# Performance work log

Measured on AMD Instinct MI355X. Metric: run time of the kernel, lower is better.

## Reference

```python
import math
import jax, jax.numpy as jnp
import numpy as np
from jax import lax

N = 224
EPS_BN = 1e-5


def _conv(x, w, b):
    y = lax.conv_general_dilated(x, w, (1, 1), 'SAME',
                                 dimension_numbers=('NCHW', 'OIHW', 'NCHW'))
    return y + b[None, :, None, None]


def _bn(x, g, beta, m, v):
    # eval-mode BatchNorm2d with running stats
    inv = lax.rsqrt(v + EPS_BN)
    return (x - m[None, :, None, None]) * (g * inv)[None, :, None, None] + beta[None, :, None, None]


def _maxpool2(x):
    return lax.reduce_window(x, -jnp.inf, lax.max, (1, 1, 2, 2), (1, 1, 2, 2), 'VALID')


def setup_inputs() -> dict:
    key = jax.random.key(0)
    ks = jax.random.split(key, 12)
    idx = np.arange(N, dtype=np.float32)
    angles = 2.0 * math.pi * idx[None, :] * idx[:, None] / N
    inp = {
        'sequences': jax.random.normal(ks[0], (16, 8, 3, N, N), dtype=jnp.float32),
        'dft_cos': jnp.asarray(np.cos(angles), dtype=jnp.float32),
        'dft_sin': jnp.asarray(np.sin(angles), dtype=jnp.float32),
        'conv1_w': jax.random.normal(ks[1], (16, 3, 3, 3), dtype=jnp.float32) * 0.1,
        'conv1_b': jnp.zeros((16,), jnp.float32),
        'bn1_g': jnp.ones((16,), jnp.float32),
        'bn1_b': jnp.zeros((16,), jnp.float32),
        'bn1_m': jnp.zeros((16,), jnp.float32),
        'bn1_v': jnp.ones((16,), jnp.float32),
        'conv2_w': jax.random.normal(ks[2], (32, 16, 3, 3), dtype=jnp.float32) * 0.05,
        'conv2_b': jnp.zeros((32,), jnp.float32),
        'bn2_g': jnp.ones((32,), jnp.float32),
        'bn2_b': jnp.zeros((32,), jnp.float32),
        'bn2_m': jnp.zeros((32,), jnp.float32),
        'bn2_v': jnp.ones((32,), jnp.float32),
        'conv3_w': jax.random.normal(ks[3], (64, 32, 3, 3), dtype=jnp.float32) * 0.05,
        'conv3_b': jnp.zeros((64,), jnp.float32),
        'bn3_g': jnp.ones((64,), jnp.float32),
        'bn3_b': jnp.zeros((64,), jnp.float32),
        'bn3_m': jnp.zeros((64,), jnp.float32),
        'bn3_v': jnp.ones((64,), jnp.float32),
        'fc_w': jax.random.normal(ks[4], (128, 64), dtype=jnp.float32) * 0.1,
        'fc_b': jnp.zeros((128,), jnp.float32),
    }
    return inp


def reference(sequences, dft_cos, dft_sin,
              conv1_w, conv1_b, bn1_g, bn1_b, bn1_m, bn1_v,
              conv2_w, conv2_b, bn2_g, bn2_b, bn2_m, bn2_v,
              conv3_w, conv3_b, bn3_g, bn3_b, bn3_m, bn3_v,
              fc_w, fc_b):
    b, s = sequences.shape[0], sequences.shape[1]
    x = sequences[:, s // 2]  # center frames [B,3,H,W]

    # 2D DFT via dense matmul chain: X = (C - jS) x (C - jS)
    C, S = dft_cos, dft_sin
    Cx = jnp.einsum('ij,bcjk->bcik', C, x)
    Sx = jnp.einsum('ij,bcjk->bcik', S, x)
    X_real = jnp.einsum('bcij,jk->bcik', Cx, C) - jnp.einsum('bcij,jk->bcik', Sx, S)
    X_imag = -(jnp.einsum('bcij,jk->bcik', Cx, S) + jnp.einsum('bcij,jk->bcik', Sx, C))
    magnitude = jnp.sqrt(X_real ** 2 + X_imag ** 2 + 1e-08)
    spec = jnp.log(magnitude + 1e-08)
    half = N // 2
    spec = jnp.roll(spec, shift=(half, half), axis=(-2, -1))  # fftshift

    # CNN stack (eval-mode BN, dropout disabled)
    h = jax.nn.relu(_bn(_conv(spec, conv1_w, conv1_b), bn1_g, bn1_b, bn1_m, bn1_v))
    h = _maxpool2(h)
    h = jax.nn.relu(_bn(_conv(h, conv2_w, conv2_b), bn2_g, bn2_b, bn2_m, bn2_v))
    h = _maxpool2(h)
    h = jax.nn.relu(_bn(_conv(h, conv3_w, conv3_b), bn3_g, bn3_b, bn3_m, bn3_v))
    h = jnp.mean(h, axis=(2, 3))  # AdaptiveAvgPool2d((1,1)) + flatten -> [B,64]

    freq_out = jax.nn.relu(h @ fc_w.T + fc_b)  # dropout = identity in eval
    return freq_out
```

## Files before the change

kernel.cpp:

```cpp
#include <hip/hip_runtime.h>
#include <math.h>
#include <stddef.h>

#define N224 224
#define PIX 50176
#define ROWS113 25312

#define OFF_SX    1214976
#define OFF_SPEC  4816896
#define OFF_WT    3211264
#define OFF_WT2   (OFF_WT + 24576)
#define OFF_WT1   (OFF_WT + 30720)
#define OFF_SU3   (OFF_WT + 31296)
#define OFF_SU2   (OFF_WT + 31424)
#define OFF_SU1   (OFF_WT + 31488)
#define OFF_PART  (OFF_WT + 32768)

__global__ __launch_bounds__(256) void prep(
    const float* __restrict__ c1w, const float* __restrict__ c2w,
    const float* __restrict__ c3w, const float* __restrict__ c1b,
    const float* __restrict__ c2b, const float* __restrict__ c3b,
    const float* __restrict__ g1, const float* __restrict__ be1,
    const float* __restrict__ m1, const float* __restrict__ v1,
    const float* __restrict__ g2, const float* __restrict__ be2,
    const float* __restrict__ m2, const float* __restrict__ v2,
    const float* __restrict__ g3, const float* __restrict__ be3,
    const float* __restrict__ m3, const float* __restrict__ v3,
    float* __restrict__ wt3, float* __restrict__ wt2, float* __restrict__ wt1,
    float* __restrict__ su3, float* __restrict__ su2, float* __restrict__ su1)
{
  const int idx = blockIdx.x * 256 + threadIdx.x;
  const int stride = gridDim.x * 256;
  for (int i = idx; i < 32*64*12; i += stride) {
    const int cc = i / 768, r = i % 768, co = r / 12, k = r % 12;
    wt3[i] = (k < 9) ? c3w[co*288 + cc*9 + k] : 0.f;
  }
  for (int i = idx; i < 16*32*12; i += stride) {
    const int cc = i / 384, r = i % 384, co = r / 12, k = r % 12;
    wt2[i] = (k < 9) ? c2w[co*144 + cc*9 + k] : 0.f;
  }
  for (int i = idx; i < 3*16*12; i += stride) {
    const int cc = i / 192, r = i % 192, co = r / 12, k = r % 12;
    wt1[i] = (k < 9) ? c1w[co*27 + cc*9 + k] : 0.f;
  }
  if (idx < 64) {
    const float s = g3[idx] * rsqrtf(v3[idx] + 1e-5f);
    su3[idx] = s; su3[64+idx] = (c3b[idx] - m3[idx]) * s + be3[idx];
  } else if (idx < 96) {
    const int c = idx - 64;
    const float s = g2[c] * rsqrtf(v2[c] + 1e-5f);
    su2[c] = s; su2[32+c] = (c2b[c] - m2[c]) * s + be2[c];
  } else if (idx < 112) {
    const int c = idx - 96;
    const float s = g1[c] * rsqrtf(v1[c] + 1e-5f);
    su1[c] = s; su1[16+c] = (c1b[c] - m1[c]) * s + be1[c];
  }
}

__global__ __launch_bounds__(256) void dft1(
    const float* __restrict__ seq, const float* __restrict__ Cm,
    const float* __restrict__ Sm, float* __restrict__ Cx, float* __restrict__ Sx)
{
  const int p = blockIdx.z;
  const int b = p / 3, ch = p % 3;
  const float* __restrict__ x = seq + ((((size_t)b * 8 + 4) * 3 + ch) * PIX);
  const int i0 = blockIdx.y * 32;
  const int k0 = blockIdx.x * 32;
  const int tid = threadIdx.x;
  const int tx = tid & 15, ty = tid >> 4;
  __shared__ float Ctt[16][36], Stt[16][36], Xt[16][36];
  float aC[2][2] = {{0,0},{0,0}}, aS[2][2] = {{0,0},{0,0}};

  const int sidx = tid & 127;
  const int srow = sidx >> 2;
  const int skq  = (sidx & 3) * 4;
  const bool isC = tid < 128;
  const float* __restrict__ csb = (isC ? Cm : Sm) + (size_t)(i0 + srow) * N224 + skq;
  const int xjr = tid >> 4;
  const int xc  = (tid & 15) * 2;
  const float* __restrict__ xb = x + (size_t)xjr * N224 + k0 + xc;

  for (int jt = 0; jt < 14; ++jt) {
    const int j = jt * 16;
    __syncthreads();
    {
      const float4 v = *(const float4*)(csb + j);
      float (*dst)[36] = isC ? Ctt : Stt;
      dst[skq+0][srow] = v.x; dst[skq+1][srow] = v.y;
      dst[skq+2][srow] = v.z; dst[skq+3][srow] = v.w;
      *(float2*)&Xt[xjr][xc] = *(const float2*)(xb + (size_t)j * N224);
    }
    __syncthreads();
#pragma unroll
    for (int jj = 0; jj < 16; ++jj) {
      const float2 cv = *(const float2*)&Ctt[jj][2*ty];
      const float2 sv = *(const float2*)&Stt[jj][2*ty];
      const float2 xv = *(const float2*)&Xt[jj][2*tx];
      aC[0][0] = fmaf(cv.x, xv.x, aC[0][0]); aC[0][1] = fmaf(cv.x, xv.y, aC[0][1]);
      aC[1][0] = fmaf(cv.y, xv.x, aC[1][0]); aC[1][1] = fmaf(cv.y, xv.y, aC[1][1]);
      aS[0][0] = fmaf(sv.x, xv.x, aS[0][0]); aS[0][1] = fmaf(sv.x, xv.y, aS[0][1]);
      aS[1][0] = fmaf(sv.y, xv.x, aS[1][0]); aS[1][1] = fmaf(sv.y, xv.y, aS[1][1]);
    }
  }
  const size_t b113 = (size_t)p * ROWS113;
#pragma unroll
  for (int a = 0; a < 2; ++a) {
    const int i = i0 + 2*ty + a;
    if (i <= 112) {
      const size_t off = b113 + (size_t)i * N224 + k0 + 2*tx;
      *(float2*)&Cx[off] = make_float2(aC[a][0], aC[a][1]);
      *(float2*)&Sx[off] = make_float2(aS[a][0], aS[a][1]);
    }
  }
}

__global__ __launch_bounds__(256) void dft2(
    const float* __restrict__ Cx, const float* __restrict__ Sx,
    const float* __restrict__ Cm, const float* __restrict__ Sm,
    float* __restrict__ spec)
{
  const int p = blockIdx.z;
  const int i0 = blockIdx.y * 32;
  const int k0 = blockIdx.x * 32;
  const int tid = threadIdx.x;
  const int tx = tid & 15, ty = tid >> 4;
  const size_t b113 = (size_t)p * ROWS113;
  __shared__ float CxT[16][36], SxT[16][36], Ct[16][36], St[16][36];
  float p1[2][2] = {{0,0},{0,0}}, p2[2][2] = {{0,0},{0,0}};
  float p3[2][2] = {{0,0},{0,0}}, p4[2][2] = {{0,0},{0,0}};

  const int sidx = tid & 127;
  const int srow = sidx >> 2;
  const int skq  = (sidx & 3) * 4;
  const bool isCx = tid < 128;
  const int ri = (i0 + srow > 112) ? 112 : i0 + srow;
  const float* __restrict__ ab = (isCx ? Cx : Sx) + b113 + (size_t)ri * N224 + skq;
  const int jr = tid >> 4;
  const int cc2 = (tid & 15) * 2;
  const float* __restrict__ cb = Cm + (size_t)jr * N224 + k0 + cc2;
  const float* __restrict__ sb2 = Sm + (size_t)jr * N224 + k0 + cc2;

  for (int jt = 0; jt < 14; ++jt) {
    const int j = jt * 16;
    __syncthreads();
    {
      const float4 v = *(const float4*)(ab + j);
      float (*dst)[36] = isCx ? CxT : SxT;
      dst[skq+0][srow] = v.x; dst[skq+1][srow] = v.y;
      dst[skq+2][srow] = v.z; dst[skq+3][srow] = v.w;
      *(float2*)&Ct[jr][cc2] = *(const float2*)(cb + (size_t)j * N224);
      *(float2*)&St[jr][cc2] = *(const float2*)(sb2 + (size_t)j * N224);
    }
    __syncthreads();
#pragma unroll
    for (int jj = 0; jj < 16; ++jj) {
      const float2 cxv = *(const float2*)&CxT[jj][2*ty];
      const float2 sxv = *(const float2*)&SxT[jj][2*ty];
      const float2 ccv = *(const float2*)&Ct[jj][2*tx];
      const float2 ssv = *(const float2*)&St[jj][2*tx];
      const float cxa[2] = {cxv.x, cxv.y};
      const float sxa[2] = {sxv.x, sxv.y};
      const float cca[2] = {ccv.x, ccv.y};
      const float ssa[2] = {ssv.x, ssv.y};
#pragma unroll
      for (int a = 0; a < 2; ++a)
#pragma unroll
        for (int d = 0; d < 2; ++d) {
          p1[a][d] = fmaf(cxa[a], cca[d], p1[a][d]);
          p2[a][d] = fmaf(sxa[a], ssa[d], p2[a][d]);
          p3[a][d] = fmaf(cxa[a], ssa[d], p3[a][d]);
          p4[a][d] = fmaf(sxa[a], cca[d], p4[a][d]);
        }
    }
  }
  const size_t sb = (size_t)p * PIX;
#pragma unroll
  for (int a = 0; a < 2; ++a) {
    const int i = i0 + 2*ty + a;
    if (i > 112) continue;
    const int shi  = (i < 112) ? i + 112 : i - 112;
    const int shmi = 112 - i;
    const bool irm = (i >= 1) && (i <= 111);
#pragma unroll
    for (int d = 0; d < 2; ++d) {
      const int k = k0 + 2*tx + d;
      if (k > 112) continue;
      const float r1 = p1[a][d] - p2[a][d];
      const float i1 = p3[a][d] + p4[a][d];
      const float sp1v = logf(sqrtf(fmaf(r1, r1, fmaf(i1, i1, 1e-8f))) + 1e-8f);
      const float r2v = p1[a][d] + p2[a][d];
      const float i2v = p3[a][d] - p4[a][d];
      const float sp2v = logf(sqrtf(fmaf(r2v, r2v, fmaf(i2v, i2v, 1e-8f))) + 1e-8f);
      const int shk  = (k < 112) ? k + 112 : k - 112;
      const int shmk = 112 - k;
      const bool krm = (k >= 1) && (k <= 111);
      spec[sb + (size_t)shi*N224 + shk] = sp1v;
      if (irm)        spec[sb + (size_t)shmi*N224 + shk ] = sp2v;
      if (krm)        spec[sb + (size_t)shi *N224 + shmk] = sp2v;
      if (irm && krm) spec[sb + (size_t)shmi*N224 + shmk] = sp1v;
    }
  }
}

__global__ __launch_bounds__(256) void conv1(
    const float* __restrict__ spec, const float* __restrict__ wt1,
    const float* __restrict__ su1, float* __restrict__ out)
{
  const int band = blockIdx.x, b = blockIdx.y;
  const int tid = threadIdx.x;
  const int lane = tid & 63, w = tid >> 6;
  const int co = lane & 15, cr = (lane >> 4) & 1, xs = lane >> 5;
  const int xh = w >> 1, xq = w & 1;
  __shared__ float in_t[3][4][232];
  for (int i = tid; i < 3*4*232; i += 256) {
    const int c = i % 232, r = (i / 232) % 4, cc = i / 928;
    const int y = band*2 - 1 + r, gx = c - 1;
    float v = 0.f;
    if (c < 226 && y >= 0 && y < 224 && gx >= 0 && gx < 224)
      v = spec[((size_t)b*3 + cc) * PIX + (size_t)y * N224 + gx];
    in_t[cc][r][c] = v;
  }
  __syncthreads();
  const int X0 = xh*112 + xq*56 + xs*28;
  float acc[28];
#pragma unroll
  for (int px = 0; px < 28; ++px) acc[px] = 0.f;
#pragma unroll
  for (int cc = 0; cc < 3; ++cc) {
    const float4 w0 = *(const float4*)&wt1[cc*192 + co*12];
    const float4 w1 = *(const float4*)&wt1[cc*192 + co*12 + 4];
    const float  w8 = wt1[cc*192 + co*12 + 8];
    const float wr[9] = {w0.x, w0.y, w0.z, w0.w, w1.x, w1.y, w1.z, w1.w, w8};
#pragma unroll
    for (int ky = 0; ky < 3; ++ky) {
      float xr[32];
      const float4* rp = (const float4*)&in_t[cc][cr + ky][X0];
#pragma unroll
      for (int t = 0; t < 8; ++t) {
        const float4 v = rp[t];
        xr[4*t]=v.x; xr[4*t+1]=v.y; xr[4*t+2]=v.z; xr[4*t+3]=v.w;
      }
#pragma unroll
      for (int px = 0; px < 28; ++px) {
        acc[px] = fmaf(xr[px  ], wr[ky*3  ], acc[px]);
        acc[px] = fmaf(xr[px+1], wr[ky*3+1], acc[px]);
        acc[px] = fmaf(xr[px+2], wr[ky*3+2], acc[px]);
      }
    }
  }
  const float s = su1[co], u = su1[16+co];
  float m[14];
#pragma unroll
  for (int p = 0; p < 14; ++p)
    m[p] = fmaxf(acc[2*p]*s + u, acc[2*p+1]*s + u);
#pragma unroll
  for (int p = 0; p < 14; ++p) {
    const float pm = __shfl_xor(m[p], 16);
    m[p] = fmaxf(fmaxf(m[p], pm), 0.f);
  }
  if (cr == 0) {
    const int pxb = X0 >> 1;
    float* op = &out[(((size_t)b*16 + co)*112 + band)*112 + pxb];
#pragma unroll
    for (int p = 0; p < 14; ++p) op[p] = m[p];
  }
}

__global__ __launch_bounds__(256) void conv2(
    const float* __restrict__ h1, const float* __restrict__ wt2,
    const float* __restrict__ su2, float* __restrict__ out)
{
  const int xh = blockIdx.x, band = blockIdx.y, b = blockIdx.z;
  const int tid = threadIdx.x;
  const int lane = tid & 63, w = tid >> 6;
  const int co = lane & 31, cr = lane >> 5;
  __shared__ float in_t[16][4][64];
  for (int i = tid; i < 16*4*58; i += 256) {
    const int c = i % 58, r = (i / 58) % 4, cc = i / 232;
    const int y = band*2 - 1 + r, gx = xh*56 - 1 + c;
    float v = 0.f;
    if (y >= 0 && y < 112 && gx >= 0 && gx < 112)
      v = h1[(((size_t)b*16 + cc)*112 + y)*112 + gx];
    in_t[cc][r][c] = v;
  }
  __syncthreads();
  const int X0 = w * 14;
  float acc[14];
#pragma unroll
  for (int px = 0; px < 14; ++px) acc[px] = 0.f;
  const float* __restrict__ wp = wt2 + co*12;
  float4 nw0 = *(const float4*)(wp);
  float4 nw1 = *(const float4*)(wp + 4);
  float  nw8 = wp[8];
  for (int cc = 0; cc < 16; ++cc) {
    const float4 w0 = nw0, w1 = nw1; const float w8 = nw8;
    if (cc < 15) {
      const float* np = wp + (cc + 1) * 384;
      nw0 = *(const float4*)(np);
      nw1 = *(const float4*)(np + 4);
      nw8 = np[8];
    }
    const float wr[9] = {w0.x, w0.y, w0.z, w0.w, w1.x, w1.y, w1.z, w1.w, w8};
#pragma unroll
    for (int ky = 0; ky < 3; ++ky) {
      float xr[16];
      const float2* rp = (const float2*)&in_t[cc][cr + ky][X0];
#pragma unroll
      for (int t = 0; t < 8; ++t) {
        const float2 v = rp[t];
        xr[2*t] = v.x; xr[2*t+1] = v.y;
      }
#pragma unroll
      for (int px = 0; px < 14; ++px) {
        acc[px] = fmaf(xr[px  ], wr[ky*3  ], acc[px]);
        acc[px] = fmaf(xr[px+1], wr[ky*3+1], acc[px]);
        acc[px] = fmaf(xr[px+2], wr[ky*3+2], acc[px]);
      }
    }
  }
  const float s = su2[co], u = su2[32+co];
  float m[7];
#pragma unroll
  for (int p = 0; p < 7; ++p)
    m[p] = fmaxf(acc[2*p]*s + u, acc[2*p+1]*s + u);
#pragma unroll
  for (int p = 0; p < 7; ++p) {
    const float pm = __shfl_xor(m[p], 32);
    m[p] = fmaxf(fmaxf(m[p], pm), 0.f);
  }
  if (cr == 0) {
    float* op = &out[(((size_t)b*32 + co)*56 + band)*56 + xh*28 + w*7];
#pragma unroll
    for (int p = 0; p < 7; ++p) op[p] = m[p];
  }
}

__global__ __launch_bounds__(256) void conv3(
    const float* __restrict__ h2, const float* __restrict__ wt3,
    const float* __restrict__ su3, float* __restrict__ part)
{
  const int band = blockIdx.x, b = blockIdx.y;
  const int tid = threadIdx.x;
  const int co = tid & 63, w = tid >> 6;
  __shared__ float in_t[32][3][64];
  __shared__ float red[4][64];
  for (int i = tid; i < 32*3*58; i += 256) {
    const int c = i % 58, r = (i / 58) % 3, cc = i / 174;
    const int y = band - 1 + r, gx = c - 1;
    float v = 0.f;
    if (y >= 0 && y < 56 && gx >= 0 && gx < 56)
      v = h2[(((size_t)b*32 + cc)*56 + y)*56 + gx];
    in_t[cc][r][c] = v;
  }
  __syncthreads();
  const int X0 = w * 14;
  float acc[14];
#pragma unroll
  for (int px = 0; px < 14; ++px) acc[px] = 0.f;
  const float* __restrict__ wp = wt3 + co*12;
  float4 nw0 = *(const float4*)(wp);
  float4 nw1 = *(const float4*)(wp + 4);
  float  nw8 = wp[8];
  for (int cc = 0; cc < 32; ++cc) {
    const float4 w0 = nw0, w1 = nw1; const float w8 = nw8;
    if (cc < 31) {
      const float* np = wp + (cc + 1) * 768;
      nw0 = *(const float4*)(np);
      nw1 = *(const float4*)(np + 4);
      nw8 = np[8];
    }
    const float wr[9] = {w0.x, w0.y, w0.z, w0.w, w1.x, w1.y, w1.z, w1.w, w8};
#pragma unroll
    for (int rr = 0; rr < 3; ++rr) {
      float xr[16];
      const float2* rp = (const float2*)&in_t[cc][rr][X0];
#pragma unroll
      for (int t = 0; t < 8; ++t) {
        const float2 v = rp[t];
        xr[2*t] = v.x; xr[2*t+1] = v.y;
      }
#pragma unroll
      for (int px = 0; px < 14; ++px) {
        acc[px] = fmaf(xr[px  ], wr[rr*3  ], acc[px]);
        acc[px] = fmaf(xr[px+1], wr[rr*3+1], acc[px]);
        acc[px] = fmaf(xr[px+2], wr[rr*3+2], acc[px]);
      }
    }
  }
  const float s = su3[co], u = su3[64+co];
  float sum = 0.f;
#pragma unroll
  for (int px = 0; px < 14; ++px)
    sum += fmaxf(acc[px]*s + u, 0.f);
  red[w][co] = sum;
  __syncthreads();
  if (tid < 64)
    part[((size_t)b*64 + co)*56 + band] =
        red[0][co] + red[1][co] + red[2][co] + red[3][co];
}

__global__ __launch_bounds__(128) void mean_fc(
    const float* __restrict__ part, const float* __restrict__ fw,
    const float* __restrict__ fb, float* __restrict__ out)
{
  const int b = blockIdx.x;
  const int tid = threadIdx.x;
  __shared__ float h3s[64];
  if (tid < 64) {
    float s = 0.f;
    const float* pp = part + ((size_t)b*64 + tid)*56;
#pragma unroll
    for (int i = 0; i < 56; ++i) s += pp[i];
    h3s[tid] = s * (1.0f / 3136.0f);
  }
  __syncthreads();
  float acc = fb[tid];
#pragma unroll
  for (int c = 0; c < 64; ++c)
    acc = fmaf(h3s[c], fw[tid*64 + c], acc);
  out[b*128 + tid] = fmaxf(acc, 0.f);
}

extern "C" void kernel_launch(void* const* d_in, const int* in_sizes, int n_in,
                              void* d_out, int out_size, void* d_ws, size_t ws_size,
                              hipStream_t stream) {
  const float* seq  = (const float*)d_in[0];
  const float* dcos = (const float*)d_in[1];
  const float* dsin = (const float*)d_in[2];
  const float* c1w  = (const float*)d_in[3];
  const float* c1b  = (const float*)d_in[4];
  const float* b1g  = (const float*)d_in[5];
  const float* b1b  = (const float*)d_in[6];
  const float* b1m  = (const float*)d_in[7];
  const float* b1v  = (const float*)d_in[8];
  const float* c2w  = (const float*)d_in[9];
  const float* c2b  = (const float*)d_in[10];
  const float* b2g  = (const float*)d_in[11];
  const float* b2b  = (const float*)d_in[12];
  const float* b2m  = (const float*)d_in[13];
  const float* b2v  = (const float*)d_in[14];
  const float* c3w  = (const float*)d_in[15];
  const float* c3b  = (const float*)d_in[16];
  const float* b3g  = (const float*)d_in[17];
  const float* b3b  = (const float*)d_in[18];
  const float* b3m  = (const float*)d_in[19];
  const float* b3v  = (const float*)d_in[20];
  const float* fw   = (const float*)d_in[21];
  const float* fb   = (const float*)d_in[22];
  float* out = (float*)d_out;

  float* ws   = (float*)d_ws;
  float* Cx   = ws;
  float* Sx   = ws + OFF_SX;
  float* spec = ws + OFF_SPEC;
  float* h1   = ws;
  float* h2   = ws + OFF_SPEC;
  float* wt3  = ws + OFF_WT;
  float* wt2  = ws + OFF_WT2;
  float* wt1  = ws + OFF_WT1;
  float* su3  = ws + OFF_SU3;
  float* su2  = ws + OFF_SU2;
  float* su1  = ws + OFF_SU1;
  float* part = ws + OFF_PART;

  prep<<<24, 256, 0, stream>>>(c1w, c2w, c3w, c1b, c2b, c3b,
                               b1g, b1b, b1m, b1v, b2g, b2b, b2m, b2v,
                               b3g, b3b, b3m, b3v, wt3, wt2, wt1, su3, su2, su1);
  dft1<<<dim3(7, 4, 48), 256, 0, stream>>>(seq, dcos, dsin, Cx, Sx);
  dft2<<<dim3(4, 4, 48), 256, 0, stream>>>(Cx, Sx, dcos, dsin, spec);
  conv1<<<dim3(112, 16), 256, 0, stream>>>(spec, wt1, su1, h1);
  conv2<<<dim3(2, 56, 16), 256, 0, stream>>>(h1, wt2, su2, h2);
  conv3<<<dim3(56, 16), 256, 0, stream>>>(h2, wt3, su3, part);
  mean_fc<<<16, 128, 0, stream>>>(part, fw, fb, out);
}
```

Baseline: 163.5 us.

## Register-block conv2 over two output rows and conv3 over two channels with half-size blocks

conv2 now computes both pooled input rows per thread, reusing each loaded shared-memory row across two output rows. This removes the cross-lane shuffle for the vertical max and halves the threads per block. conv3 gives each thread two output channels, so each loaded input row feeds twice as many FMAs, and block size drops to 128 with a shuffle-based reduction. The cost is more live registers per thread and fewer threads per block, which may lower occupancy and latency hiding.

Result: slower. 172.8 us (+5.7%).

```diff
diff --git a/kernel.cpp b/kernel.cpp
--- a/kernel.cpp
+++ b/kernel.cpp
@@ -266,16 +266,16 @@
   }
 }
 
-__global__ __launch_bounds__(256) void conv2(
+__global__ __launch_bounds__(128) void conv2(
     const float* __restrict__ h1, const float* __restrict__ wt2,
     const float* __restrict__ su2, float* __restrict__ out)
 {
   const int xh = blockIdx.x, band = blockIdx.y, b = blockIdx.z;
   const int tid = threadIdx.x;
   const int lane = tid & 63, w = tid >> 6;
-  const int co = lane & 31, cr = lane >> 5;
-  __shared__ float in_t[16][4][64];
-  for (int i = tid; i < 16*4*58; i += 256) {
+  const int co = lane & 31, xs = lane >> 5;
+  __shared__ float in_t[16][4][60];
+  for (int i = tid; i < 16*4*58; i += 128) {
     const int c = i % 58, r = (i / 58) % 4, cc = i / 232;
     const int y = band*2 - 1 + r, gx = xh*56 - 1 + c;
     float v = 0.f;
@@ -284,10 +284,12 @@
     in_t[cc][r][c] = v;
   }
   __syncthreads();
-  const int X0 = w * 14;
-  float acc[14];
-#pragma unroll
-  for (int px = 0; px < 14; ++px) acc[px] = 0.f;
+  const int X0 = w*28 + xs*14;
+  float acc[2][14];
+#pragma unroll
+  for (int r = 0; r < 2; ++r)
+#pragma unroll
+    for (int px = 0; px < 14; ++px) acc[r][px] = 0.f;
   const float* __restrict__ wp = wt2 + co*12;
   float4 nw0 = *(const float4*)(wp);
   float4 nw1 = *(const float4*)(wp + 4);
@@ -302,49 +304,48 @@
     }
     const float wr[9] = {w0.x, w0.y, w0.z, w0.w, w1.x, w1.y, w1.z, w1.w, w8};
 #pragma unroll
-    for (int ky = 0; ky < 3; ++ky) {
+    for (int rr = 0; rr < 4; ++rr) {
       float xr[16];
-      const float2* rp = (const float2*)&in_t[cc][cr + ky][X0];
+      const float2* rp = (const float2*)&in_t[cc][rr][X0];
 #pragma unroll
       for (int t = 0; t < 8; ++t) {
         const float2 v = rp[t];
         xr[2*t] = v.x; xr[2*t+1] = v.y;
       }
 #pragma unroll
-      for (int px = 0; px < 14; ++px) {
-        acc[px] = fmaf(xr[px  ], wr[ky*3  ], acc[px]);
-        acc[px] = fmaf(xr[px+1], wr[ky*3+1], acc[px]);
-        acc[px] = fmaf(xr[px+2], wr[ky*3+2], acc[px]);
+      for (int crow = 0; crow < 2; ++crow) {
+        const int ky = rr - crow;
+        if (ky < 0 || ky > 2) continue;
+#pragma unroll
+        for (int px = 0; px < 14; ++px) {
+          acc[crow][px] = fmaf(xr[px  ], wr[ky*3  ], acc[crow][px]);
+          acc[crow][px] = fmaf(xr[px+1], wr[ky*3+1], acc[crow][px]);
+          acc[crow][px] = fmaf(xr[px+2], wr[ky*3+2], acc[crow][px]);
+        }
       }
     }
   }
   const float s = su2[co], u = su2[32+co];
-  float m[7];
-#pragma unroll
-  for (int p = 0; p < 7; ++p)
-    m[p] = fmaxf(acc[2*p]*s + u, acc[2*p+1]*s + u);
+  float* op = &out[(((size_t)b*32 + co)*56 + band)*56 + xh*28 + w*14 + xs*7];
 #pragma unroll
   for (int p = 0; p < 7; ++p) {
-    const float pm = __shfl_xor(m[p], 32);
-    m[p] = fmaxf(fmaxf(m[p], pm), 0.f);
-  }
-  if (cr == 0) {
-    float* op = &out[(((size_t)b*32 + co)*56 + band)*56 + xh*28 + w*7];
-#pragma unroll
-    for (int p = 0; p < 7; ++p) op[p] = m[p];
-  }
-}
-
-__global__ __launch_bounds__(256) void conv3(
+    const float v0 = acc[0][2*p]*s + u,   v1 = acc[0][2*p+1]*s + u;
+    const float v2 = acc[1][2*p]*s + u,   v3 = acc[1][2*p+1]*s + u;
+    op[p] = fmaxf(fmaxf(fmaxf(v0, v1), fmaxf(v2, v3)), 0.f);
+  }
+}
+
+__global__ __launch_bounds__(128) void conv3(
     const float* __restrict__ h2, const float* __restrict__ wt3,
     const float* __restrict__ su3, float* __restrict__ part)
 {
   const int band = blockIdx.x, b = blockIdx.y;
   const int tid = threadIdx.x;
-  const int co = tid & 63, w = tid >> 6;
-  __shared__ float in_t[32][3][64];
-  __shared__ float red[4][64];
-  for (int i = tid; i < 32*3*58; i += 256) {
+  const int lane = tid & 63, w = tid >> 6;
+  const int co = lane & 31, xs = lane >> 5;
+  __shared__ float in_t[32][3][60];
+  __shared__ float red[2][64];
+  for (int i = tid; i < 32*3*58; i += 128) {
     const int c = i % 58, r = (i / 58) % 3, cc = i / 174;
     const int y = band - 1 + r, gx = c - 1;
     float v = 0.f;
@@ -353,23 +354,29 @@
     in_t[cc][r][c] = v;
   }
   __syncthreads();
-  const int X0 = w * 14;
-  float acc[14];
-#pragma unroll
-  for (int px = 0; px < 14; ++px) acc[px] = 0.f;
-  const float* __restrict__ wp = wt3 + co*12;
-  float4 nw0 = *(const float4*)(wp);
-  float4 nw1 = *(const float4*)(wp + 4);
-  float  nw8 = wp[8];
+  const int X0 = w*28 + xs*14;
+  float accA[14], accB[14];
+#pragma unroll
+  for (int px = 0; px < 14; ++px) { accA[px] = 0.f; accB[px] = 0.f; }
+  const float* __restrict__ wpA = wt3 + co*12;
+  const float* __restrict__ wpB = wt3 + (co + 32)*12;
+  float4 nA0 = *(const float4*)(wpA);
+  float4 nA1 = *(const float4*)(wpA + 4);
+  float  nA8 = wpA[8];
+  float4 nB0 = *(const float4*)(wpB);
+  float4 nB1 = *(const float4*)(wpB + 4);
+  float  nB8 = wpB[8];
   for (int cc = 0; cc < 32; ++cc) {
-    const float4 w0 = nw0, w1 = nw1; const float w8 = nw8;
+    const float4 a0 = nA0, a1 = nA1; const float a8 = nA8;
+    const float4 b0 = nB0, b1 = nB1; const float b8 = nB8;
     if (cc < 31) {
-      const float* np = wp + (cc + 1) * 768;
-      nw0 = *(const float4*)(np);
-      nw1 = *(const float4*)(np + 4);
-      nw8 = np[8];
-    }
-    const float wr[9] = {w0.x, w0.y, w0.z, w0.w, w1.x, w1.y, w1.z, w1.w, w8};
+      const float* npA = wpA + (cc + 1) * 768;
+      const float* npB = wpB + (cc + 1) * 768;
+      nA0 = *(const float4*)(npA); nA1 = *(const float4*)(npA + 4); nA8 = npA[8];
+      nB0 = *(const float4*)(npB); nB1 = *(const float4*)(npB + 4); nB8 = npB[8];
+    }
+    const float wA[9] = {a0.x, a0.y, a0.z, a0.w, a1.x, a1.y, a1.z, a1.w, a8};
+    const float wB[9] = {b0.x, b0.y, b0.z, b0.w, b1.x, b1.y, b1.z, b1.w, b8};
 #pragma unroll
     for (int rr = 0; rr < 3; ++rr) {
       float xr[16];
@@ -381,22 +388,32 @@
       }
 #pragma unroll
       for (int px = 0; px < 14; ++px) {
-        acc[px] = fmaf(xr[px  ], wr[rr*3  ], acc[px]);
-        acc[px] = fmaf(xr[px+1], wr[rr*3+1], acc[px]);
-        acc[px] = fmaf(xr[px+2], wr[rr*3+2], acc[px]);
-      }
-    }
-  }
-  const float s = su3[co], u = su3[64+co];
-  float sum = 0.f;
-#pragma unroll
-  for (int px = 0; px < 14; ++px)
-    sum += fmaxf(acc[px]*s + u, 0.f);
-  red[w][co] = sum;
+        accA[px] = fmaf(xr[px  ], wA[rr*3  ], accA[px]);
+        accA[px] = fmaf(xr[px+1], wA[rr*3+1], accA[px]);
+        accA[px] = fmaf(xr[px+2], wA[rr*3+2], accA[px]);
+        accB[px] = fmaf(xr[px  ], wB[rr*3  ], accB[px]);
+        accB[px] = fmaf(xr[px+1], wB[rr*3+1], accB[px]);
+        accB[px] = fmaf(xr[px+2], wB[rr*3+2], accB[px]);
+      }
+    }
+  }
+  const float sA = su3[co],    uA = su3[64+co];
+  const float sB = su3[co+32], uB = su3[96+co];
+  float sumA = 0.f, sumB = 0.f;
+#pragma unroll
+  for (int px = 0; px < 14; ++px) {
+    sumA += fmaxf(accA[px]*sA + uA, 0.f);
+    sumB += fmaxf(accB[px]*sB + uB, 0.f);
+  }
+  sumA += __shfl_xor(sumA, 32);
+  sumB += __shfl_xor(sumB, 32);
+  if (xs == 0) {
+    red[w][co]      = sumA;
+    red[w][co + 32] = sumB;
+  }
   __syncthreads();
   if (tid < 64)
-    part[((size_t)b*64 + co)*56 + band] =
-        red[0][co] + red[1][co] + red[2][co] + red[3][co];
+    part[((size_t)b*64 + tid)*56 + band] = red[0][tid] + red[1][tid];
 }
 
 __global__ __launch_bounds__(128) void mean_fc(
@@ -469,7 +486,7 @@
   dft1<<<dim3(7, 4, 48), 256, 0, stream>>>(seq, dcos, dsin, Cx, Sx);
   dft2<<<dim3(4, 4, 48), 256, 0, stream>>>(Cx, Sx, dcos, dsin, spec);
   conv1<<<dim3(112, 16), 256, 0, stream>>>(spec, wt1, su1, h1);
-  conv2<<<dim3(2, 56, 16), 256, 0, stream>>>(h1, wt2, su2, h2);
-  conv3<<<dim3(56, 16), 256, 0, stream>>>(h2, wt3, su3, part);
+  conv2<<<dim3(2, 56, 16), 128, 0, stream>>>(h1, wt2, su2, h2);
+  conv3<<<dim3(56, 16), 128, 0, stream>>>(h2, wt3, su3, part);
   mean_fc<<<16, 128, 0, stream>>>(part, fw, fb, out);
 }
```
